# Optimization experiments

Hardware: AMD Instinct MI355X
Metric: run time of the kernel (lower is better)

Reference implementation:

```python
import jax, jax.numpy as jnp
import numpy as np
from jax import lax

BN_EPS = 1e-5


def _conv_block(x, w, b):
    # conv k=3 pad=1 (NCHW), relu, maxpool 2x2 stride 2 (floor)
    y = lax.conv_general_dilated(x, w, (1, 1), [(1, 1), (1, 1)],
                                 dimension_numbers=('NCHW', 'OIHW', 'NCHW'))
    y = jax.nn.relu(y + b[None, :, None, None])
    y = lax.reduce_window(y, -jnp.inf, lax.max, (1, 1, 2, 2), (1, 1, 2, 2), 'VALID')
    return y


def _batchnorm_train(x, g, b):
    # BatchNorm2d in train mode: biased batch stats over (N,H,W)
    m = jnp.mean(x, axis=(0, 2, 3), keepdims=True)
    v = jnp.mean(jnp.square(x - m), axis=(0, 2, 3), keepdims=True)
    return g[None, :, None, None] * (x - m) * lax.rsqrt(v + BN_EPS) + b[None, :, None, None]


def setup_inputs() -> dict:
    key = jax.random.key(0)
    ks = jax.random.split(key, 16)
    B = 4096
    s = lambda k, shape, fan: jax.random.normal(k, shape, jnp.float32) * (1.0 / np.sqrt(fan))
    return {
        'x':   jax.random.normal(ks[0], (B, 1, 28, 28), jnp.float32),
        'cw1': s(ks[1], (32, 1, 3, 3), 9),    'cb1': jnp.zeros((32,), jnp.float32),
        'cw2': s(ks[2], (32, 32, 3, 3), 288), 'cb2': jnp.zeros((32,), jnp.float32),
        'cw3': s(ks[3], (32, 32, 3, 3), 288), 'cb3': jnp.zeros((32,), jnp.float32),
        'bn_g': jnp.ones((32,), jnp.float32), 'bn_b': jnp.zeros((32,), jnp.float32),
        'pw1': s(ks[4], (288, 128), 288), 'pb1': jnp.zeros((128,), jnp.float32),
        'pw2': s(ks[5], (128, 128), 128), 'pb2': jnp.zeros((128,), jnp.float32),
        'pw3': s(ks[6], (128, 3), 128),   'pb3': jnp.zeros((3,), jnp.float32),
        'ew1': s(ks[7], (3, 288, 128), 288), 'eb1': jnp.zeros((3, 128), jnp.float32),
        'ew2': s(ks[8], (3, 128, 128), 128), 'eb2': jnp.zeros((3, 128), jnp.float32),
        'ew3': s(ks[9], (3, 128, 10), 128),  'eb3': jnp.zeros((3, 10), jnp.float32),
    }


def _select_linear(h, oh, ew, eb):
    # per-example expert Linear: compute all 3 tiny experts, pick via one-hot
    y = jnp.einsum('bi,eio->beo', h, ew) + eb[None]  # [B,3,out]
    return jnp.einsum('beo,be->bo', y, oh)


def reference(x, cw1, cb1, cw2, cb2, cw3, cb3, bn_g, bn_b,
              pw1, pb1, pw2, pb2, pw3, pb3,
              ew1, eb1, ew2, eb2, ew3, eb3):
    # conv stack
    y = _conv_block(x, cw1, cb1)
    y = _conv_block(y, cw2, cb2)
    y = _conv_block(y, cw3, cb3)
    y = _batchnorm_train(y, bn_g, bn_b)
    y = y.reshape(y.shape[0], -1)  # [B, 288]

    # ActorCritic approx policy MLP (288 -> 128 -> 128 -> 3), greedy action
    h = jax.nn.relu(y @ pw1 + pb1)
    h = jax.nn.relu(h @ pw2 + pb2)
    logits = h @ pw3 + pb3
    actions = jnp.argmax(logits, axis=-1)          # [B] int, routing decision
    oh = jax.nn.one_hot(actions, 3, dtype=y.dtype)  # [B,3]

    # three SelectionLayers, same per-example routing decision
    y = _select_linear(y, oh, ew1, eb1)
    y = _select_linear(y, oh, ew2, eb2)
    y = _select_linear(y, oh, ew3, eb3)  # [B,10]
    return y, actions
```

## Files before the change

### kernel.cpp

```cpp
#include <hip/hip_runtime.h>

__global__ __launch_bounds__(256) void repack_kernel(
    const float* __restrict__ cw2, const float* __restrict__ cw3,
    float* __restrict__ packed2, float* __restrict__ packed3)
{
    int t = blockIdx.x * 256 + threadIdx.x;
    if (t < 9216) {
        int oc = t & 31, r = t >> 5;
        packed2[t] = cw2[oc * 288 + r];
    } else {
        int t2 = t - 9216;
        int oc = t2 & 31, r = t2 >> 5;
        packed3[t2] = cw3[oc * 288 + r];
    }
}

__global__ __launch_bounds__(256)
void fused_conv_kernel(
    const float* __restrict__ x,
    const float* __restrict__ cw1, const float* __restrict__ cb1,
    const float* __restrict__ packed2, const float* __restrict__ cb2,
    const float* __restrict__ packed3, const float* __restrict__ cb3,
    float* __restrict__ out3, float* __restrict__ gstats)
{
    const int img = blockIdx.x;
    const int tid = threadIdx.x;

    __shared__ float A[1220];
    __shared__ float B[8320];
    __shared__ float b2s[32], b3s[32];

    float* xs1  = A;
    float* w1s  = A + 900;
    float* b1s  = A + 1188;
    float* wck2 = A;
    float* xs2  = B;
    float* sc   = B;
    float* xs3  = B + 1280;
    float* wck3 = B + 4160;
    float* sc2  = B + 5073;

    for (int i = tid; i < 900;  i += 256) xs1[i] = 0.f;
    for (int i = tid; i < 8320; i += 256) B[i] = 0.f;
    __syncthreads();

    for (int i = tid; i < 784; i += 256) {
        int yy = i / 28, xx = i % 28;
        xs1[(yy + 1) * 30 + xx + 1] = x[img * 784 + i];
    }
    for (int i = tid; i < 288; i += 256) {
        int oc = i & 31, tap = i >> 5;
        w1s[i] = cw1[oc * 9 + tap];
    }
    if (tid < 32) { b1s[tid] = cb1[tid]; b2s[tid] = cb2[tid]; b3s[tid] = cb3[tid]; }
    __syncthreads();

    {
        const int c1 = tid & 31;
        float w1r[9];
        #pragma unroll
        for (int t = 0; t < 9; t++) w1r[t] = w1s[t * 32 + c1];
        const float bias1 = b1s[c1];
        for (int o = tid; o < 32 * 196; o += 256) {
            int p = o >> 5;
            int py = p / 14, px = p % 14;
            int base = (2 * py) * 30 + 2 * px;
            float P[16];
            #pragma unroll
            for (int r = 0; r < 4; r++) {
                float2 u0 = *(const float2*)&xs1[base + r * 30];
                float2 u1 = *(const float2*)&xs1[base + r * 30 + 2];
                P[r * 4 + 0] = u0.x; P[r * 4 + 1] = u0.y;
                P[r * 4 + 2] = u1.x; P[r * 4 + 3] = u1.y;
            }
            float a00 = 0.f, a01 = 0.f, a10 = 0.f, a11 = 0.f;
            #pragma unroll
            for (int ky = 0; ky < 3; ky++)
                #pragma unroll
                for (int kx = 0; kx < 3; kx++) {
                    float w = w1r[ky * 3 + kx];
                    a00 = fmaf(P[ky * 4 + kx],           w, a00);
                    a01 = fmaf(P[ky * 4 + kx + 1],       w, a01);
                    a10 = fmaf(P[(ky + 1) * 4 + kx],     w, a10);
                    a11 = fmaf(P[(ky + 1) * 4 + kx + 1], w, a11);
                }
            float v = fmaxf(fmaxf(fmaxf(a00, a01), fmaxf(a10, a11)) + bias1, 0.f);
            int r = py + 1, col = px + 1;
            xs2[c1 * 260 + r * 16 + ((((col >> 2) + r) & 3) << 2) + (col & 3)] = v;
        }
    }

    const int g  = tid >> 7;
    const int u  = tid & 127;
    const int cb = u & 7, R = u >> 3;
    const int oc0 = cb * 4;
    const bool act2 = (u < 112);

    float acc[4][14];
    #pragma unroll
    for (int a = 0; a < 4; a++)
        #pragma unroll
        for (int c = 0; c < 14; c++) acc[a][c] = 0.f;

    float pf[5];
    #pragma unroll
    for (int k = 0; k < 5; k++) {
        int idx = tid + k * 256;
        pf[k] = (idx < 1152) ? packed2[idx] : 0.f;
    }

    for (int ch = 0; ch < 8; ch++) {
        __syncthreads();
        #pragma unroll
        for (int k = 0; k < 5; k++) {
            int idx = tid + k * 256;
            if (idx < 1152) wck2[idx] = pf[k];
        }
        if (ch < 7) {
            #pragma unroll
            for (int k = 0; k < 5; k++) {
                int idx = tid + k * 256;
                pf[k] = (idx < 1152) ? packed2[(ch + 1) * 1152 + idx] : 0.f;
            }
        }
        __syncthreads();
        if (act2) {
            #pragma unroll
            for (int d = 0; d < 2; d++) {
                const int ld = g * 2 + d;
                const int ic = ch * 4 + ld;
                const float* wd = &wck2[ld * 288 + oc0];
                const int pb = ic * 260;
                #pragma unroll
                for (int ky = 0; ky < 3; ky++) {
                    const int rp = R + ky;
                    const int rb = pb + rp * 16;
                    float row[16];
                    #pragma unroll
                    for (int q = 0; q < 4; q++) {
                        const float4 t = *(const float4*)&xs2[rb + (((q + rp) & 3) << 2)];
                        row[q * 4 + 0] = t.x; row[q * 4 + 1] = t.y;
                        row[q * 4 + 2] = t.z; row[q * 4 + 3] = t.w;
                    }
                    const float4 wa = *(const float4*)&wd[(ky * 3 + 0) * 32];
                    const float4 wb = *(const float4*)&wd[(ky * 3 + 1) * 32];
                    const float4 wc = *(const float4*)&wd[(ky * 3 + 2) * 32];
                    #pragma unroll
                    for (int c = 0; c < 14; c++) {
                        acc[0][c] = fmaf(row[c],     wa.x, acc[0][c]);
                        acc[1][c] = fmaf(row[c],     wa.y, acc[1][c]);
                        acc[2][c] = fmaf(row[c],     wa.z, acc[2][c]);
                        acc[3][c] = fmaf(row[c],     wa.w, acc[3][c]);
                        acc[0][c] = fmaf(row[c + 1], wb.x, acc[0][c]);
                        acc[1][c] = fmaf(row[c + 1], wb.y, acc[1][c]);
                        acc[2][c] = fmaf(row[c + 1], wb.z, acc[2][c]);
                        acc[3][c] = fmaf(row[c + 1], wb.w, acc[3][c]);
                        acc[0][c] = fmaf(row[c + 2], wc.x, acc[0][c]);
                        acc[1][c] = fmaf(row[c + 2], wc.y, acc[1][c]);
                        acc[2][c] = fmaf(row[c + 2], wc.z, acc[2][c]);
                        acc[3][c] = fmaf(row[c + 2], wc.w, acc[3][c]);
                    }
                }
            }
        }
    }

    __syncthreads();
    if (g == 1 && act2) {
        #pragma unroll
        for (int a = 0; a < 4; a++)
            #pragma unroll
            for (int c = 0; c < 14; c++) sc[u * 57 + a * 14 + c] = acc[a][c];
    }
    __syncthreads();
    if (g == 0 && act2) {
        #pragma unroll
        for (int a = 0; a < 4; a++)
            #pragma unroll
            for (int c = 0; c < 14; c++) acc[a][c] += sc[u * 57 + a * 14 + c];
    }
    __syncthreads();

    for (int i = tid; i < 2880; i += 256) xs3[i] = 0.f;
    float hm[4][7];
    if (g == 0 && act2) {
        #pragma unroll
        for (int a = 0; a < 4; a++)
            #pragma unroll
            for (int c = 0; c < 7; c++)
                hm[a][c] = fmaxf(acc[a][2 * c], acc[a][2 * c + 1]);
        if (R & 1) {
            #pragma unroll
            for (int a = 0; a < 4; a++)
                #pragma unroll
                for (int c = 0; c < 7; c++) sc2[u * 29 + a * 7 + c] = hm[a][c];
        }
    }
    __syncthreads();
    if (g == 0 && act2 && !(R & 1)) {
        const int py = R >> 1;
        #pragma unroll
        for (int a = 0; a < 4; a++)
            #pragma unroll
            for (int c = 0; c < 7; c++) {
                float v = fmaxf(hm[a][c], sc2[(u + 8) * 29 + a * 7 + c]);
                v = fmaxf(v + b2s[oc0 + a], 0.f);
                xs3[(oc0 + a) * 90 + (py + 1) * 10 + (c + 1)] = v;
            }
    }

    const int w3v = tid >> 6;
    const int l3  = tid & 63;
    int g3, u3;
    bool act3;
    if (w3v < 2)      { g3 = w3v;       u3 = l3;            act3 = true;      }
    else if (w3v == 2){ g3 = (l3 >= 8); u3 = 64 + (l3 & 7); act3 = (l3 < 16); }
    else              { g3 = 0;         u3 = 0;             act3 = false;     }
    const int cq3 = u3 & 7, pos = u3 >> 3;
    const int oc30 = cq3 * 4;
    const int py3 = pos / 3, px3 = pos % 3;
    const int base3 = (2 * py3) * 10 + 2 * px3;

    float a3[4][4];
    #pragma unroll
    for (int a = 0; a < 4; a++)
        #pragma unroll
        for (int q = 0; q < 4; q++) a3[a][q] = 0.f;

    float pg[9];
    #pragma unroll
    for (int k = 0; k < 9; k++) pg[k] = packed3[tid + k * 256];

    for (int ch = 0; ch < 4; ch++) {
        __syncthreads();
        #pragma unroll
        for (int k = 0; k < 9; k++) wck3[tid + k * 256] = pg[k];
        if (ch < 3) {
            #pragma unroll
            for (int k = 0; k < 9; k++) pg[k] = packed3[(ch + 1) * 2304 + tid + k * 256];
        }
        __syncthreads();
        if (act3) {
            #pragma unroll 2
            for (int d = 0; d < 4; d++) {
                const int ld = g3 * 4 + d;
                const int ic = ch * 8 + ld;
                const float* xp = &xs3[ic * 90 + base3];
                float P[16];
                #pragma unroll
                for (int r = 0; r < 4; r++) {
                    float2 u0 = *(const float2*)&xp[r * 10];
                    float2 u1 = *(const float2*)&xp[r * 10 + 2];
                    P[r * 4 + 0] = u0.x; P[r * 4 + 1] = u0.y;
                    P[r * 4 + 2] = u1.x; P[r * 4 + 3] = u1.y;
                }
                const float* wd = &wck3[ld * 288 + oc30];
                #pragma unroll
                for (int tap = 0; tap < 9; tap++) {
                    const int ky = tap / 3, kx = tap % 3;
                    const float4 wv = *(const float4*)&wd[tap * 32];
                    const float x00 = P[ky * 4 + kx];
                    const float x01 = P[ky * 4 + kx + 1];
                    const float x10 = P[(ky + 1) * 4 + kx];
                    const float x11 = P[(ky + 1) * 4 + kx + 1];
                    a3[0][0] = fmaf(x00, wv.x, a3[0][0]); a3[0][1] = fmaf(x01, wv.x, a3[0][1]);
                    a3[0][2] = fmaf(x10, wv.x, a3[0][2]); a3[0][3] = fmaf(x11, wv.x, a3[0][3]);
                    a3[1][0] = fmaf(x00, wv.y, a3[1][0]); a3[1][1] = fmaf(x01, wv.y, a3[1][1]);
                    a3[1][2] = fmaf(x10, wv.y, a3[1][2]); a3[1][3] = fmaf(x11, wv.y, a3[1][3]);
                    a3[2][0] = fmaf(x00, wv.z, a3[2][0]); a3[2][1] = fmaf(x01, wv.z, a3[2][1]);
                    a3[2][2] = fmaf(x10, wv.z, a3[2][2]); a3[2][3] = fmaf(x11, wv.z, a3[2][3]);
                    a3[3][0] = fmaf(x00, wv.w, a3[3][0]); a3[3][1] = fmaf(x01, wv.w, a3[3][1]);
                    a3[3][2] = fmaf(x10, wv.w, a3[3][2]); a3[3][3] = fmaf(x11, wv.w, a3[3][3]);
                }
            }
        }
    }

    __syncthreads();
    if (g3 == 1 && act3) {
        #pragma unroll
        for (int a = 0; a < 4; a++)
            #pragma unroll
            for (int q = 0; q < 4; q++) sc[u3 * 17 + a * 4 + q] = a3[a][q];
    }
    __syncthreads();
    float rres[4];
    const bool writer = (g3 == 0 && act3);
    if (writer) {
        #pragma unroll
        for (int a = 0; a < 4; a++)
            #pragma unroll
            for (int q = 0; q < 4; q++) a3[a][q] += sc[u3 * 17 + a * 4 + q];
        float4 res;
        #pragma unroll
        for (int a = 0; a < 4; a++) {
            float v = fmaxf(fmaxf(a3[a][0], a3[a][1]), fmaxf(a3[a][2], a3[a][3]));
            rres[a] = fmaxf(v + b3s[oc30 + a], 0.f);
        }
        res.x = rres[0]; res.y = rres[1]; res.z = rres[2]; res.w = rres[3];
        *(float4*)&out3[img * 288 + pos * 32 + oc30] = res;
    }

    __syncthreads();
    for (int i = tid; i < 576; i += 256) B[i] = 0.f;
    __syncthreads();
    if (writer) {
        #pragma unroll
        for (int a = 0; a < 4; a++) {
            B[pos * 64 + oc30 + a]      = rres[a];
            B[pos * 64 + 32 + oc30 + a] = rres[a] * rres[a];
        }
    }
    __syncthreads();
    if (tid < 64) {
        int c = tid & 31, part = tid >> 5;
        float s = 0.f;
        #pragma unroll
        for (int p = 0; p < 9; p++) s += B[p * 64 + part * 32 + c];
        atomicAdd(&gstats[part * 32 + c], s);
    }
}

__global__ __launch_bounds__(512) void mlp_select_kernel(
    const float* __restrict__ out3, const float* __restrict__ gstats,
    const float* __restrict__ bng, const float* __restrict__ bnb,
    const float* __restrict__ pw1, const float* __restrict__ pb1,
    const float* __restrict__ pw2, const float* __restrict__ pb2,
    const float* __restrict__ pw3, const float* __restrict__ pb3,
    const float* __restrict__ ew1, const float* __restrict__ eb1,
    const float* __restrict__ ew2, const float* __restrict__ eb2,
    const float* __restrict__ ew3, const float* __restrict__ eb3,
    float* __restrict__ out)
{
    const int tid = threadIdx.x;
    const int img0 = blockIdx.x * 8;

    __shared__ float ysT[288 * 14];
    __shared__ float hAT[128 * 14];
    __shared__ float hBT[128 * 14];
    __shared__ float wst[32 * 128];
    __shared__ float lgp[48];
    __shared__ float sp[160];
    __shared__ int   acts[8];
    __shared__ float sa[32], sb[32];

    if (tid < 32) {
        float S = gstats[tid], SS = gstats[32 + tid];
        const float inv_n = 1.f / (4096.f * 9.f);
        float mean = S * inv_n;
        float var = SS * inv_n - mean * mean;
        float a = bng[tid] * rsqrtf(var + 1e-5f);
        sa[tid] = a;
        sb[tid] = bnb[tid] - a * mean;
    }
    __syncthreads();

    for (int it = 0; it < 2; it++) {
        int i4 = it * 512 + tid;
        if (i4 < 576) {
            int e = i4 / 72, jq = i4 - e * 72;
            float4 v = *(const float4*)&out3[(img0 + e) * 288 + jq * 4];
            int j = jq * 4;
            ysT[(j + 0) * 14 + e] = fmaf(sa[(j + 0) & 31], v.x, sb[(j + 0) & 31]);
            ysT[(j + 1) * 14 + e] = fmaf(sa[(j + 1) & 31], v.y, sb[(j + 1) & 31]);
            ysT[(j + 2) * 14 + e] = fmaf(sa[(j + 2) & 31], v.z, sb[(j + 2) & 31]);
            ysT[(j + 3) * 14 + e] = fmaf(sa[(j + 3) & 31], v.w, sb[(j + 3) & 31]);
        }
    }

    const int kg = tid >> 8;
    const int t8 = tid & 255;
    const int n4 = t8 & 31;
    const int eE = t8 >> 5;
    const int j0 = kg * 16;
    float acc[4];

    {
        acc[0] = 0.f; acc[1] = 0.f; acc[2] = 0.f; acc[3] = 0.f;
        for (int t = 0; t < 9; t++) {
            __syncthreads();
            #pragma unroll
            for (int s = 0; s < 2; s++) {
                int idx = s * 512 + tid;
                int row = idx >> 5, c4 = idx & 31;
                int k = t * 32 + row;
                int i = (k & 31) * 9 + (k >> 5);
                *(float4*)&wst[row * 128 + c4 * 4] =
                    *(const float4*)&pw1[i * 128 + c4 * 4];
            }
            __syncthreads();
            #pragma unroll
            for (int j = 0; j < 16; j++) {
                float4 w = *(const float4*)&wst[(j0 + j) * 128 + n4 * 4];
                float yv = ysT[(t * 32 + j0 + j) * 14 + eE];
                acc[0] = fmaf(yv, w.x, acc[0]); acc[1] = fmaf(yv, w.y, acc[1]);
                acc[2] = fmaf(yv, w.z, acc[2]); acc[3] = fmaf(yv, w.w, acc[3]);
            }
        }
        __syncthreads();
        if (kg) *(float4*)&wst[t8 * 4] = make_float4(acc[0], acc[1], acc[2], acc[3]);
        __syncthreads();
        if (!kg) {
            float4 p = *(const float4*)&wst[t8 * 4];
            float4 b = *(const float4*)&pb1[n4 * 4];
            hAT[(n4 * 4 + 0) * 14 + eE] = fmaxf(acc[0] + p.x + b.x, 0.f);
            hAT[(n4 * 4 + 1) * 14 + eE] = fmaxf(acc[1] + p.y + b.y, 0.f);
            hAT[(n4 * 4 + 2) * 14 + eE] = fmaxf(acc[2] + p.z + b.z, 0.f);
            hAT[(n4 * 4 + 3) * 14 + eE] = fmaxf(acc[3] + p.w + b.w, 0.f);
        }
    }

    {
        acc[0] = 0.f; acc[1] = 0.f; acc[2] = 0.f; acc[3] = 0.f;
        for (int t = 0; t < 4; t++) {
            __syncthreads();
            #pragma unroll
            for (int s = 0; s < 2; s++) {
                int idx = s * 512 + tid;
                int row = idx >> 5, c4 = idx & 31;
                int k = t * 32 + row;
                *(float4*)&wst[row * 128 + c4 * 4] =
                    *(const float4*)&pw2[k * 128 + c4 * 4];
            }
            __syncthreads();
            #pragma unroll
            for (int j = 0; j < 16; j++) {
                float4 w = *(const float4*)&wst[(j0 + j) * 128 + n4 * 4];
                float hv = hAT[(t * 32 + j0 + j) * 14 + eE];
                acc[0] = fmaf(hv, w.x, acc[0]); acc[1] = fmaf(hv, w.y, acc[1]);
                acc[2] = fmaf(hv, w.z, acc[2]); acc[3] = fmaf(hv, w.w, acc[3]);
            }
        }
        __syncthreads();
        if (kg) *(float4*)&wst[t8 * 4] = make_float4(acc[0], acc[1], acc[2], acc[3]);
        __syncthreads();
        if (!kg) {
            float4 p = *(const float4*)&wst[t8 * 4];
            float4 b = *(const float4*)&pb2[n4 * 4];
            hBT[(n4 * 4 + 0) * 14 + eE] = fmaxf(acc[0] + p.x + b.x, 0.f);
            hBT[(n4 * 4 + 1) * 14 + eE] = fmaxf(acc[1] + p.y + b.y, 0.f);
            hBT[(n4 * 4 + 2) * 14 + eE] = fmaxf(acc[2] + p.z + b.z, 0.f);
            hBT[(n4 * 4 + 3) * 14 + eE] = fmaxf(acc[3] + p.w + b.w, 0.f);
        }
    }
    __syncthreads();

    if (tid < 48) {
        int pr = tid & 1, eo = tid >> 1;
        int e = eo / 3, o = eo - e * 3;
        float s = pr ? 0.f : pb3[o];
        const int k0 = pr * 64;
        for (int k = k0; k < k0 + 64; k++) s = fmaf(hBT[k * 14 + e], pw3[k * 3 + o], s);
        lgp[tid] = s;
    }
    __syncthreads();
    if (tid < 8) {
        float l0 = lgp[(tid * 3 + 0) * 2] + lgp[(tid * 3 + 0) * 2 + 1];
        float l1 = lgp[(tid * 3 + 1) * 2] + lgp[(tid * 3 + 1) * 2 + 1];
        float l2 = lgp[(tid * 3 + 2) * 2] + lgp[(tid * 3 + 2) * 2 + 1];
        int a = 0; float best = l0;
        if (l1 > best) { best = l1; a = 1; }
        if (l2 > best) { best = l2; a = 2; }
        acts[tid] = a;
        out[4096 * 10 + img0 + tid] = (float)a;
    }
    __syncthreads();

    const int a = acts[eE];

    {
        const float* wb = ew1 + a * 36864;
        acc[0] = 0.f; acc[1] = 0.f; acc[2] = 0.f; acc[3] = 0.f;
        const int kb = kg * 144;
        for (int kk = 0; kk < 144; kk++) {
            int k = kb + kk;
            int i = (k & 31) * 9 + (k >> 5);
            float4 w = *(const float4*)&wb[i * 128 + n4 * 4];
            float yv = ysT[k * 14 + eE];
            acc[0] = fmaf(yv, w.x, acc[0]); acc[1] = fmaf(yv, w.y, acc[1]);
            acc[2] = fmaf(yv, w.z, acc[2]); acc[3] = fmaf(yv, w.w, acc[3]);
        }
        __syncthreads();
        if (kg) *(float4*)&wst[t8 * 4] = make_float4(acc[0], acc[1], acc[2], acc[3]);
        __syncthreads();
        if (!kg) {
            float4 p = *(const float4*)&wst[t8 * 4];
            float4 b = *(const float4*)&eb1[a * 128 + n4 * 4];
            hAT[(n4 * 4 + 0) * 14 + eE] = acc[0] + p.x + b.x;
            hAT[(n4 * 4 + 1) * 14 + eE] = acc[1] + p.y + b.y;
            hAT[(n4 * 4 + 2) * 14 + eE] = acc[2] + p.z + b.z;
            hAT[(n4 * 4 + 3) * 14 + eE] = acc[3] + p.w + b.w;
        }
    }
    __syncthreads();

    {
        const float* wb = ew2 + a * 16384;
        acc[0] = 0.f; acc[1] = 0.f; acc[2] = 0.f; acc[3] = 0.f;
        const int kb = kg * 64;
        for (int kk = 0; kk < 64; kk++) {
            int k = kb + kk;
            float4 w = *(const float4*)&wb[k * 128 + n4 * 4];
            float hv = hAT[k * 14 + eE];
            acc[0] = fmaf(hv, w.x, acc[0]); acc[1] = fmaf(hv, w.y, acc[1]);
            acc[2] = fmaf(hv, w.z, acc[2]); acc[3] = fmaf(hv, w.w, acc[3]);
        }
        __syncthreads();
        if (kg) *(float4*)&wst[t8 * 4] = make_float4(acc[0], acc[1], acc[2], acc[3]);
        __syncthreads();
        if (!kg) {
            float4 p = *(const float4*)&wst[t8 * 4];
            float4 b = *(const float4*)&eb2[a * 128 + n4 * 4];
            hBT[(n4 * 4 + 0) * 14 + eE] = acc[0] + p.x + b.x;
            hBT[(n4 * 4 + 1) * 14 + eE] = acc[1] + p.y + b.y;
            hBT[(n4 * 4 + 2) * 14 + eE] = acc[2] + p.z + b.z;
            hBT[(n4 * 4 + 3) * 14 + eE] = acc[3] + p.w + b.w;
        }
    }
    __syncthreads();

    if (tid < 160) {
        int pr = (tid >= 80) ? 1 : 0;
        int idx = tid - pr * 80;
        int e = idx / 10, o = idx - e * 10;
        int aa = acts[e];
        const float* w3 = &ew3[aa * 1280];
        float s = pr ? 0.f : eb3[aa * 10 + o];
        const int k0 = pr * 64;
        for (int k = k0; k < k0 + 64; k++) s = fmaf(hBT[k * 14 + e], w3[k * 10 + o], s);
        sp[tid] = s;
    }
    __syncthreads();
    if (tid < 80) {
        int e = tid / 10, o = tid - e * 10;
        out[(img0 + e) * 10 + o] = sp[tid] + sp[tid + 80];
    }
}

extern "C" void kernel_launch(void* const* d_in, const int* in_sizes, int n_in,
                              void* d_out, int out_size, void* d_ws, size_t ws_size,
                              hipStream_t stream)
{
    const float* x   = (const float*)d_in[0];
    const float* cw1 = (const float*)d_in[1];
    const float* cb1 = (const float*)d_in[2];
    const float* cw2 = (const float*)d_in[3];
    const float* cb2 = (const float*)d_in[4];
    const float* cw3 = (const float*)d_in[5];
    const float* cb3 = (const float*)d_in[6];
    const float* bng = (const float*)d_in[7];
    const float* bnb = (const float*)d_in[8];
    const float* pw1 = (const float*)d_in[9];
    const float* pb1 = (const float*)d_in[10];
    const float* pw2 = (const float*)d_in[11];
    const float* pb2 = (const float*)d_in[12];
    const float* pw3 = (const float*)d_in[13];
    const float* pb3 = (const float*)d_in[14];
    const float* ew1 = (const float*)d_in[15];
    const float* eb1 = (const float*)d_in[16];
    const float* ew2 = (const float*)d_in[17];
    const float* eb2 = (const float*)d_in[18];
    const float* ew3 = (const float*)d_in[19];
    const float* eb3 = (const float*)d_in[20];

    float* out     = (float*)d_out;
    float* out3    = (float*)d_ws;
    float* gstats  = out3 + 4096 * 288;
    float* packed2 = gstats + 64;
    float* packed3 = packed2 + 9216;

    hipMemsetAsync(gstats, 0, 64 * sizeof(float), stream);
    repack_kernel<<<72, 256, 0, stream>>>(cw2, cw3, packed2, packed3);
    fused_conv_kernel<<<4096, 256, 0, stream>>>(x, cw1, cb1, packed2, cb2,
                                                packed3, cb3, out3, gstats);
    mlp_select_kernel<<<512, 512, 0, stream>>>(out3, gstats, bng, bnb,
                                               pw1, pb1, pw2, pb2, pw3, pb3,
                                               ew1, eb1, ew2, eb2, ew3, eb3, out);
}
```

Before: 411.4 us.

## Group examples by routed expert and run expert layers in grouped blocks

The old fused MLP+select kernel is split in two. The policy kernel computes the argmax and scatters each example index into a per-expert bucket using atomic counters. A small prefix kernel then computes per-expert block offsets. A grouped select kernel processes 16 same-expert examples per block and stages the expert weights in LDS tiles with register prefetch. This is meant to stop every thread doing scattered per-example expert-weight loads and to reuse each weight tile across 16 examples. It adds two extra launches, a dependency on the atomic bucket counts, and a fixed grid of 258 blocks where surplus blocks exit early.

```diff
diff --git a/kernel.cpp b/kernel.cpp
--- a/kernel.cpp
+++ b/kernel.cpp
@@ -321,15 +321,13 @@
     }
 }
 
-__global__ __launch_bounds__(512) void mlp_select_kernel(
+__global__ __launch_bounds__(512) void mlp_argmax_kernel(
     const float* __restrict__ out3, const float* __restrict__ gstats,
     const float* __restrict__ bng, const float* __restrict__ bnb,
     const float* __restrict__ pw1, const float* __restrict__ pb1,
     const float* __restrict__ pw2, const float* __restrict__ pb2,
     const float* __restrict__ pw3, const float* __restrict__ pb3,
-    const float* __restrict__ ew1, const float* __restrict__ eb1,
-    const float* __restrict__ ew2, const float* __restrict__ eb2,
-    const float* __restrict__ ew3, const float* __restrict__ eb3,
+    int* __restrict__ cntg, int* __restrict__ idxbuf,
     float* __restrict__ out)
 {
     const int tid = threadIdx.x;
@@ -340,9 +338,9 @@
     __shared__ float hBT[128 * 14];
     __shared__ float wst[32 * 128];
     __shared__ float lgp[48];
-    __shared__ float sp[160];
     __shared__ int   acts[8];
     __shared__ float sa[32], sb[32];
+    __shared__ int   lcnt[3], lbase[3];
 
     if (tid < 32) {
         float S = gstats[tid], SS = gstats[32 + tid];
@@ -452,8 +450,11 @@
         const int k0 = pr * 64;
         for (int k = k0; k < k0 + 64; k++) s = fmaf(hBT[k * 14 + e], pw3[k * 3 + o], s);
         lgp[tid] = s;
-    }
-    __syncthreads();
+    } else if (tid < 51) {
+        lcnt[tid - 48] = 0;
+    }
+    __syncthreads();
+    int tk = 0;
     if (tid < 8) {
         float l0 = lgp[(tid * 3 + 0) * 2] + lgp[(tid * 3 + 0) * 2 + 1];
         float l1 = lgp[(tid * 3 + 1) * 2] + lgp[(tid * 3 + 1) * 2 + 1];
@@ -463,77 +464,205 @@
         if (l2 > best) { best = l2; a = 2; }
         acts[tid] = a;
         out[4096 * 10 + img0 + tid] = (float)a;
-    }
-    __syncthreads();
-
-    const int a = acts[eE];
+        tk = atomicAdd(&lcnt[a], 1);
+    }
+    __syncthreads();
+    if (tid < 3) lbase[tid] = atomicAdd(&cntg[tid], lcnt[tid]);
+    __syncthreads();
+    if (tid < 8) {
+        int a = acts[tid];
+        idxbuf[a * 4096 + lbase[a] + tk] = img0 + tid;
+    }
+}
+
+__global__ void prefix_kernel(const int* __restrict__ cntg, int* __restrict__ blkoff)
+{
+    if (threadIdx.x == 0) {
+        int n0 = (cntg[0] + 15) >> 4;
+        int n1 = (cntg[1] + 15) >> 4;
+        int n2 = (cntg[2] + 15) >> 4;
+        blkoff[0] = 0;
+        blkoff[1] = n0;
+        blkoff[2] = n0 + n1;
+        blkoff[3] = n0 + n1 + n2;
+    }
+}
+
+__global__ __launch_bounds__(512) void select_grouped_kernel(
+    const float* __restrict__ out3, const float* __restrict__ gstats,
+    const float* __restrict__ bng, const float* __restrict__ bnb,
+    const float* __restrict__ ew1, const float* __restrict__ eb1,
+    const float* __restrict__ ew2, const float* __restrict__ eb2,
+    const float* __restrict__ ew3, const float* __restrict__ eb3,
+    const int* __restrict__ cntg, const int* __restrict__ blkoff,
+    const int* __restrict__ idxbuf,
+    float* __restrict__ out)
+{
+    const int tid = threadIdx.x;
+    const int b = blockIdx.x;
+
+    const int bo1 = blkoff[1], bo2 = blkoff[2], bo3 = blkoff[3];
+    if (b >= bo3) return;
+    int a, chunk;
+    if (b < bo1)      { a = 0; chunk = b; }
+    else if (b < bo2) { a = 1; chunk = b - bo1; }
+    else              { a = 2; chunk = b - bo2; }
+
+    __shared__ float ysT[288 * 18];
+    __shared__ float hAT[128 * 18];
+    __shared__ float hBT[128 * 18];
+    __shared__ float wtile[64 * 128];
+    __shared__ float sp[320];
+    __shared__ float sa[32], sb[32];
+    __shared__ int   gidx[16];
+
+    const int cnt = cntg[a];
+    const int s0 = chunk * 16;
+
+    if (tid < 32) {
+        float S = gstats[tid], SS = gstats[32 + tid];
+        const float inv_n = 1.f / (4096.f * 9.f);
+        float mean = S * inv_n;
+        float var = SS * inv_n - mean * mean;
+        float aa = bng[tid] * rsqrtf(var + 1e-5f);
+        sa[tid] = aa;
+        sb[tid] = bnb[tid] - aa * mean;
+    }
+    if (tid < 16) {
+        int s = s0 + tid;
+        gidx[tid] = idxbuf[a * 4096 + (s < cnt ? s : cnt - 1)];
+    }
+    __syncthreads();
+
+    for (int it = 0; it < 3; it++) {
+        int i4 = it * 512 + tid;
+        if (i4 < 1152) {
+            int e = i4 / 72, jq = i4 - e * 72;
+            float4 v = *(const float4*)&out3[gidx[e] * 288 + jq * 4];
+            int j = jq * 4;
+            ysT[(j + 0) * 18 + e] = fmaf(sa[(j + 0) & 31], v.x, sb[(j + 0) & 31]);
+            ysT[(j + 1) * 18 + e] = fmaf(sa[(j + 1) & 31], v.y, sb[(j + 1) & 31]);
+            ysT[(j + 2) * 18 + e] = fmaf(sa[(j + 2) & 31], v.z, sb[(j + 2) & 31]);
+            ysT[(j + 3) * 18 + e] = fmaf(sa[(j + 3) & 31], v.w, sb[(j + 3) & 31]);
+        }
+    }
+
+    const int n4 = tid & 31;
+    const int eE = tid >> 5;
+    float acc0, acc1, acc2, acc3;
 
     {
         const float* wb = ew1 + a * 36864;
-        acc[0] = 0.f; acc[1] = 0.f; acc[2] = 0.f; acc[3] = 0.f;
-        const int kb = kg * 144;
-        for (int kk = 0; kk < 144; kk++) {
-            int k = kb + kk;
-            int i = (k & 31) * 9 + (k >> 5);
-            float4 w = *(const float4*)&wb[i * 128 + n4 * 4];
-            float yv = ysT[k * 14 + eE];
-            acc[0] = fmaf(yv, w.x, acc[0]); acc[1] = fmaf(yv, w.y, acc[1]);
-            acc[2] = fmaf(yv, w.z, acc[2]); acc[3] = fmaf(yv, w.w, acc[3]);
-        }
-        __syncthreads();
-        if (kg) *(float4*)&wst[t8 * 4] = make_float4(acc[0], acc[1], acc[2], acc[3]);
-        __syncthreads();
-        if (!kg) {
-            float4 p = *(const float4*)&wst[t8 * 4];
-            float4 b = *(const float4*)&eb1[a * 128 + n4 * 4];
-            hAT[(n4 * 4 + 0) * 14 + eE] = acc[0] + p.x + b.x;
-            hAT[(n4 * 4 + 1) * 14 + eE] = acc[1] + p.y + b.y;
-            hAT[(n4 * 4 + 2) * 14 + eE] = acc[2] + p.z + b.z;
-            hAT[(n4 * 4 + 3) * 14 + eE] = acc[3] + p.w + b.w;
-        }
-    }
-    __syncthreads();
+        float4 bb = *(const float4*)&eb1[a * 128 + n4 * 4];
+        acc0 = bb.x; acc1 = bb.y; acc2 = bb.z; acc3 = bb.w;
+
+        float4 pfw[4];
+        #pragma unroll
+        for (int s = 0; s < 4; s++) {
+            int slot = s * 512 + tid;
+            int row = slot >> 5, c4 = slot & 31;
+            int i = (row & 31) * 9 + (row >> 5);
+            pfw[s] = *(const float4*)&wb[i * 128 + c4 * 4];
+        }
+
+        for (int t = 0; t < 5; t++) {
+            const int rows = (t < 4) ? 64 : 32;
+            __syncthreads();
+            #pragma unroll
+            for (int s = 0; s < 4; s++) {
+                int slot = s * 512 + tid;
+                if (slot < rows * 32) {
+                    int row = slot >> 5, c4 = slot & 31;
+                    *(float4*)&wtile[row * 128 + c4 * 4] = pfw[s];
+                }
+            }
+            if (t < 4) {
+                const int nrows = (t < 3) ? 64 : 32;
+                #pragma unroll
+                for (int s = 0; s < 4; s++) {
+                    int slot = s * 512 + tid;
+                    if (slot < nrows * 32) {
+                        int row = slot >> 5, c4 = slot & 31;
+                        int k = (t + 1) * 64 + row;
+                        int i = (k & 31) * 9 + (k >> 5);
+                        pfw[s] = *(const float4*)&wb[i * 128 + c4 * 4];
+                    }
+                }
+            }
+            __syncthreads();
+            const int kb = t * 64;
+            for (int r = 0; r < rows; r++) {
+                float4 w = *(const float4*)&wtile[r * 128 + n4 * 4];
+                float yv = ysT[(kb + r) * 18 + eE];
+                acc0 = fmaf(yv, w.x, acc0); acc1 = fmaf(yv, w.y, acc1);
+                acc2 = fmaf(yv, w.z, acc2); acc3 = fmaf(yv, w.w, acc3);
+            }
+        }
+        hAT[(n4 * 4 + 0) * 18 + eE] = acc0;
+        hAT[(n4 * 4 + 1) * 18 + eE] = acc1;
+        hAT[(n4 * 4 + 2) * 18 + eE] = acc2;
+        hAT[(n4 * 4 + 3) * 18 + eE] = acc3;
+    }
 
     {
         const float* wb = ew2 + a * 16384;
-        acc[0] = 0.f; acc[1] = 0.f; acc[2] = 0.f; acc[3] = 0.f;
-        const int kb = kg * 64;
-        for (int kk = 0; kk < 64; kk++) {
-            int k = kb + kk;
-            float4 w = *(const float4*)&wb[k * 128 + n4 * 4];
-            float hv = hAT[k * 14 + eE];
-            acc[0] = fmaf(hv, w.x, acc[0]); acc[1] = fmaf(hv, w.y, acc[1]);
-            acc[2] = fmaf(hv, w.z, acc[2]); acc[3] = fmaf(hv, w.w, acc[3]);
-        }
-        __syncthreads();
-        if (kg) *(float4*)&wst[t8 * 4] = make_float4(acc[0], acc[1], acc[2], acc[3]);
-        __syncthreads();
-        if (!kg) {
-            float4 p = *(const float4*)&wst[t8 * 4];
-            float4 b = *(const float4*)&eb2[a * 128 + n4 * 4];
-            hBT[(n4 * 4 + 0) * 14 + eE] = acc[0] + p.x + b.x;
-            hBT[(n4 * 4 + 1) * 14 + eE] = acc[1] + p.y + b.y;
-            hBT[(n4 * 4 + 2) * 14 + eE] = acc[2] + p.z + b.z;
-            hBT[(n4 * 4 + 3) * 14 + eE] = acc[3] + p.w + b.w;
-        }
-    }
-    __syncthreads();
-
+        float4 bb = *(const float4*)&eb2[a * 128 + n4 * 4];
+        acc0 = bb.x; acc1 = bb.y; acc2 = bb.z; acc3 = bb.w;
+
+        float4 pfw[4];
+        #pragma unroll
+        for (int s = 0; s < 4; s++) {
+            int slot = s * 512 + tid;
+            int row = slot >> 5, c4 = slot & 31;
+            pfw[s] = *(const float4*)&wb[row * 128 + c4 * 4];
+        }
+
+        for (int t = 0; t < 2; t++) {
+            __syncthreads();
+            #pragma unroll
+            for (int s = 0; s < 4; s++) {
+                int slot = s * 512 + tid;
+                int row = slot >> 5, c4 = slot & 31;
+                *(float4*)&wtile[row * 128 + c4 * 4] = pfw[s];
+            }
+            if (t < 1) {
+                #pragma unroll
+                for (int s = 0; s < 4; s++) {
+                    int slot = s * 512 + tid;
+                    int row = slot >> 5, c4 = slot & 31;
+                    pfw[s] = *(const float4*)&wb[(64 + row) * 128 + c4 * 4];
+                }
+            }
+            __syncthreads();
+            const int kb = t * 64;
+            for (int r = 0; r < 64; r++) {
+                float4 w = *(const float4*)&wtile[r * 128 + n4 * 4];
+                float hv = hAT[(kb + r) * 18 + eE];
+                acc0 = fmaf(hv, w.x, acc0); acc1 = fmaf(hv, w.y, acc1);
+                acc2 = fmaf(hv, w.z, acc2); acc3 = fmaf(hv, w.w, acc3);
+            }
+        }
+        hBT[(n4 * 4 + 0) * 18 + eE] = acc0;
+        hBT[(n4 * 4 + 1) * 18 + eE] = acc1;
+        hBT[(n4 * 4 + 2) * 18 + eE] = acc2;
+        hBT[(n4 * 4 + 3) * 18 + eE] = acc3;
+    }
+    __syncthreads();
+
+    if (tid < 320) {
+        int pr = (tid >= 160) ? 1 : 0;
+        int idx = tid - pr * 160;
+        int e = idx / 10, o = idx - e * 10;
+        const float* w3 = &ew3[a * 1280];
+        float s = pr ? 0.f : eb3[a * 10 + o];
+        const int k0 = pr * 64;
+        for (int k = k0; k < k0 + 64; k++) s = fmaf(hBT[k * 18 + e], w3[k * 10 + o], s);
+        sp[tid] = s;
+    }
+    __syncthreads();
     if (tid < 160) {
-        int pr = (tid >= 80) ? 1 : 0;
-        int idx = tid - pr * 80;
-        int e = idx / 10, o = idx - e * 10;
-        int aa = acts[e];
-        const float* w3 = &ew3[aa * 1280];
-        float s = pr ? 0.f : eb3[aa * 10 + o];
-        const int k0 = pr * 64;
-        for (int k = k0; k < k0 + 64; k++) s = fmaf(hBT[k * 14 + e], w3[k * 10 + o], s);
-        sp[tid] = s;
-    }
-    __syncthreads();
-    if (tid < 80) {
         int e = tid / 10, o = tid - e * 10;
-        out[(img0 + e) * 10 + o] = sp[tid] + sp[tid + 80];
+        if (s0 + e < cnt) out[gidx[e] * 10 + o] = sp[tid] + sp[tid + 160];
     }
 }
 
@@ -566,14 +695,21 @@
     float* out     = (float*)d_out;
     float* out3    = (float*)d_ws;
     float* gstats  = out3 + 4096 * 288;
-    float* packed2 = gstats + 64;
+    int*   cntg    = (int*)(gstats + 64);
+    int*   blkoff  = cntg + 3;
+    float* packed2 = gstats + 80;
     float* packed3 = packed2 + 9216;
-
-    hipMemsetAsync(gstats, 0, 64 * sizeof(float), stream);
+    int*   idxbuf  = (int*)(packed3 + 9216);
+
+    hipMemsetAsync(gstats, 0, 67 * sizeof(float), stream);
     repack_kernel<<<72, 256, 0, stream>>>(cw2, cw3, packed2, packed3);
     fused_conv_kernel<<<4096, 256, 0, stream>>>(x, cw1, cb1, packed2, cb2,
                                                 packed3, cb3, out3, gstats);
-    mlp_select_kernel<<<512, 512, 0, stream>>>(out3, gstats, bng, bnb,
+    mlp_argmax_kernel<<<512, 512, 0, stream>>>(out3, gstats, bng, bnb,
                                                pw1, pb1, pw2, pb2, pw3, pb3,
-                                               ew1, eb1, ew2, eb2, ew3, eb3, out);
+                                               cntg, idxbuf, out);
+    prefix_kernel<<<1, 64, 0, stream>>>(cntg, blkoff);
+    select_grouped_kernel<<<258, 512, 0, stream>>>(out3, gstats, bng, bnb,
+                                                   ew1, eb1, ew2, eb2, ew3, eb3,
+                                                   cntg, blkoff, idxbuf, out);
 }
```

New measurement: 448.7 us. 1.09x slower.

## Double weight tile depth in MLP and sort images by expert

Applied to the files above, without the earlier changes.

The policy MLP weight staging tile grows from 32 to 64 rows. This halves the number of load/sync rounds for the first two linear layers, at the cost of more shared memory per block. Images in each block are also permuted so those routed to the same expert sit in adjacent warps. That should make the per-expert weight loads more uniform within a wave, in exchange for a small sort and an extra indirection.

```diff
diff --git a/kernel.cpp b/kernel.cpp
--- a/kernel.cpp
+++ b/kernel.cpp
@@ -338,10 +338,11 @@
     __shared__ float ysT[288 * 14];
     __shared__ float hAT[128 * 14];
     __shared__ float hBT[128 * 14];
-    __shared__ float wst[32 * 128];
+    __shared__ float wst[64 * 128];
     __shared__ float lgp[48];
     __shared__ float sp[160];
     __shared__ int   acts[8];
+    __shared__ int   perm[8];
     __shared__ float sa[32], sb[32];
 
     if (tid < 32) {
@@ -372,27 +373,30 @@
     const int t8 = tid & 255;
     const int n4 = t8 & 31;
     const int eE = t8 >> 5;
-    const int j0 = kg * 16;
     float acc[4];
 
     {
         acc[0] = 0.f; acc[1] = 0.f; acc[2] = 0.f; acc[3] = 0.f;
-        for (int t = 0; t < 9; t++) {
+        for (int t = 0; t < 5; t++) {
+            const int rows = (t < 4) ? 64 : 32;
             __syncthreads();
             #pragma unroll
-            for (int s = 0; s < 2; s++) {
+            for (int s = 0; s < 4; s++) {
                 int idx = s * 512 + tid;
-                int row = idx >> 5, c4 = idx & 31;
-                int k = t * 32 + row;
-                int i = (k & 31) * 9 + (k >> 5);
-                *(float4*)&wst[row * 128 + c4 * 4] =
-                    *(const float4*)&pw1[i * 128 + c4 * 4];
+                if (idx < rows * 32) {
+                    int row = idx >> 5, c4 = idx & 31;
+                    int k = t * 64 + row;
+                    int i = (k & 31) * 9 + (k >> 5);
+                    *(float4*)&wst[row * 128 + c4 * 4] =
+                        *(const float4*)&pw1[i * 128 + c4 * 4];
+                }
             }
             __syncthreads();
-            #pragma unroll
-            for (int j = 0; j < 16; j++) {
-                float4 w = *(const float4*)&wst[(j0 + j) * 128 + n4 * 4];
-                float yv = ysT[(t * 32 + j0 + j) * 14 + eE];
+            const int jc = rows >> 1;
+            const int jb = kg * jc;
+            for (int j = 0; j < jc; j++) {
+                float4 w = *(const float4*)&wst[(jb + j) * 128 + n4 * 4];
+                float yv = ysT[(t * 64 + jb + j) * 14 + eE];
                 acc[0] = fmaf(yv, w.x, acc[0]); acc[1] = fmaf(yv, w.y, acc[1]);
                 acc[2] = fmaf(yv, w.z, acc[2]); acc[3] = fmaf(yv, w.w, acc[3]);
             }
@@ -412,21 +416,21 @@
 
     {
         acc[0] = 0.f; acc[1] = 0.f; acc[2] = 0.f; acc[3] = 0.f;
-        for (int t = 0; t < 4; t++) {
+        for (int t = 0; t < 2; t++) {
             __syncthreads();
             #pragma unroll
-            for (int s = 0; s < 2; s++) {
+            for (int s = 0; s < 4; s++) {
                 int idx = s * 512 + tid;
                 int row = idx >> 5, c4 = idx & 31;
-                int k = t * 32 + row;
+                int k = t * 64 + row;
                 *(float4*)&wst[row * 128 + c4 * 4] =
                     *(const float4*)&pw2[k * 128 + c4 * 4];
             }
             __syncthreads();
-            #pragma unroll
-            for (int j = 0; j < 16; j++) {
-                float4 w = *(const float4*)&wst[(j0 + j) * 128 + n4 * 4];
-                float hv = hAT[(t * 32 + j0 + j) * 14 + eE];
+            const int jb = kg * 32;
+            for (int j = 0; j < 32; j++) {
+                float4 w = *(const float4*)&wst[(jb + j) * 128 + n4 * 4];
+                float hv = hAT[(t * 64 + jb + j) * 14 + eE];
                 acc[0] = fmaf(hv, w.x, acc[0]); acc[1] = fmaf(hv, w.y, acc[1]);
                 acc[2] = fmaf(hv, w.z, acc[2]); acc[3] = fmaf(hv, w.w, acc[3]);
             }
@@ -466,7 +470,17 @@
     }
     __syncthreads();
 
-    const int a = acts[eE];
+    if (tid < 8) {
+        int my = acts[tid] * 8 + tid;
+        int r = 0;
+        #pragma unroll
+        for (int e2 = 0; e2 < 8; e2++) r += ((acts[e2] * 8 + e2) < my) ? 1 : 0;
+        perm[r] = tid;
+    }
+    __syncthreads();
+
+    const int pE = perm[eE];
+    const int a = acts[pE];
 
     {
         const float* wb = ew1 + a * 36864;
@@ -476,7 +490,7 @@
             int k = kb + kk;
             int i = (k & 31) * 9 + (k >> 5);
             float4 w = *(const float4*)&wb[i * 128 + n4 * 4];
-            float yv = ysT[k * 14 + eE];
+            float yv = ysT[k * 14 + pE];
             acc[0] = fmaf(yv, w.x, acc[0]); acc[1] = fmaf(yv, w.y, acc[1]);
             acc[2] = fmaf(yv, w.z, acc[2]); acc[3] = fmaf(yv, w.w, acc[3]);
         }
@@ -523,7 +537,7 @@
         int pr = (tid >= 80) ? 1 : 0;
         int idx = tid - pr * 80;
         int e = idx / 10, o = idx - e * 10;
-        int aa = acts[e];
+        int aa = acts[perm[e]];
         const float* w3 = &ew3[aa * 1280];
         float s = pr ? 0.f : eb3[aa * 10 + o];
         const int k0 = pr * 64;
@@ -533,7 +547,7 @@
     __syncthreads();
     if (tid < 80) {
         int e = tid / 10, o = tid - e * 10;
-        out[(img0 + e) * 10 + o] = sp[tid] + sp[tid + 80];
+        out[(img0 + perm[e]) * 10 + o] = sp[tid] + sp[tid + 80];
     }
 }
 
```

New measurement: 425.0 us. +3.3%, slower.
